# Performance work log

Hardware: AMD Instinct MI355X
Metric: run time of the kernel (lower is better)

Reference implementation:

```python
import jax, jax.numpy as jnp
import numpy as np

NUM_USER = 100000
NUM_ITEM = 50000
N = NUM_USER + NUM_ITEM
DIM_FEAT = 512
DIM_LATENT = 64
NNZ = 2400000
N_LAYERS = 3


def setup_inputs() -> dict:
    key = jax.random.key(0)
    ks = jax.random.split(key, 6)
    features = jax.random.normal(ks[0], (NUM_ITEM, DIM_FEAT), dtype=jnp.float32)
    user_id_preference = jax.random.normal(ks[1], (NUM_USER, DIM_LATENT), dtype=jnp.float32)
    W = jax.random.normal(ks[2], (DIM_FEAT, DIM_LATENT), dtype=jnp.float32) * (1.0 / np.sqrt(DIM_FEAT))
    b = jnp.zeros((DIM_LATENT,), dtype=jnp.float32)
    rows = jax.random.randint(ks[3], (NNZ,), 0, N, dtype=jnp.int32)
    cols = jax.random.randint(ks[4], (NNZ,), 0, N, dtype=jnp.int32)
    vals = jax.random.uniform(ks[5], (NNZ,), dtype=jnp.float32)
    return {"features": features, "user_id_preference": user_id_preference,
            "W": W, "b": b, "rows": rows, "cols": cols, "vals": vals}


def reference(features, user_id_preference, W, b, rows, cols, vals):
    # MLP projection of item features: [num_item, dim_latent]
    temp_features = features @ W + b
    # Concat user preferences and projected item features: [N, dim_latent]
    all_emb = jnp.concatenate([user_id_preference, temp_features], axis=0)
    # F.normalize: row-wise L2 normalization with eps=1e-12
    nrm = jnp.sqrt(jnp.sum(all_emb * all_emb, axis=1, keepdims=True))
    all_emb = all_emb / jnp.maximum(nrm, 1e-12)
    # 3-layer sparse propagation: out[r] += v * emb[c]; accumulate layer mean
    embs_sum = all_emb
    for _ in range(N_LAYERS):
        gathered = all_emb[cols] * vals[:, None]  # [nnz, dim_latent]
        all_emb = jax.ops.segment_sum(gathered, rows, num_segments=N)
        embs_sum = embs_sum + all_emb
    light_out = embs_sum / (N_LAYERS + 1)
    users = light_out[:NUM_USER]
    items = light_out[NUM_USER:]
    return (users, items)
```

## Files before the change

kernel.cpp:

```cpp
#include <hip/hip_runtime.h>

#define NUSER 100000
#define NITEM 50000
#define NTOT  150000
#define DF    512
#define DL    64
#define NNZ_  2400000
#define NB    1172
#define NCHUNK 256
#define CHUNK  9375

typedef short bf16x8 __attribute__((ext_vector_type(8)));
typedef float f32x4  __attribute__((ext_vector_type(4)));

__device__ __forceinline__ unsigned short bf16r(float f) {
    unsigned u = __float_as_uint(f);
    return (unsigned short)((u + 0x7FFFu + ((u >> 16) & 1u)) >> 16);
}
__device__ __forceinline__ unsigned pack2(float lo, float hi) {
    return (unsigned)bf16r(lo) | ((unsigned)bf16r(hi) << 16);
}

__global__ __launch_bounds__(256) void k_init(const float* __restrict__ up,
                                              const float* __restrict__ W,
                                              unsigned short* __restrict__ e0,
                                              unsigned short* __restrict__ Wtb) {
    int b = blockIdx.x;
    if (b < 128) {
        int idx = b * 256 + threadIdx.x;
        int k = idx >> 6, d = idx & 63;
        Wtb[d * DF + k] = bf16r(W[idx]);
        return;
    }
    int t = (b - 128) * 256 + threadIdx.x;
    float v = up[t];
    float ss = v * v;
    #pragma unroll
    for (int m = 32; m >= 1; m >>= 1) ss += __shfl_xor(ss, m, 64);
    float scale = 1.0f / fmaxf(sqrtf(ss), 1e-12f);
    e0[t] = bf16r(v * scale);
}

__global__ __launch_bounds__(256) void k_item(const float* __restrict__ F,
                                              const unsigned short* __restrict__ Wtb,
                                              const float* __restrict__ B,
                                              unsigned short* __restrict__ e0) {
    int t = threadIdx.x;
    int w = t >> 6, lane = t & 63;
    int g = lane >> 4;
    int c = lane & 15;
    int row_base = blockIdx.x * 64 + w * 16;

    int ar = row_base + c;
    if (ar >= NITEM) ar = NITEM - 1;
    const float* Frow = F + (size_t)ar * DF;

    f32x4 acc[4] = {};
    #pragma unroll 2
    for (int kc = 0; kc < DF; kc += 32) {
        int k0 = kc + g * 8;
        float4 f0 = *(const float4*)&Frow[k0];
        float4 f1 = *(const float4*)&Frow[k0 + 4];
        union { uint4 u; bf16x8 v; } a;
        a.u.x = pack2(f0.x, f0.y);
        a.u.y = pack2(f0.z, f0.w);
        a.u.z = pack2(f1.x, f1.y);
        a.u.w = pack2(f1.z, f1.w);
        #pragma unroll
        for (int ct = 0; ct < 4; ++ct) {
            union { uint4 u; bf16x8 v; } bb;
            bb.u = *(const uint4*)&Wtb[(size_t)(ct * 16 + c) * DF + k0];
            acc[ct] = __builtin_amdgcn_mfma_f32_16x16x32_bf16(a.v, bb.v, acc[ct], 0, 0, 0);
        }
    }

    #pragma unroll
    for (int ct = 0; ct < 4; ++ct) {
        float bc = B[ct * 16 + c];
        #pragma unroll
        for (int r = 0; r < 4; ++r) acc[ct][r] += bc;
    }
    float ssv[4];
    #pragma unroll
    for (int r = 0; r < 4; ++r) {
        float s = acc[0][r] * acc[0][r] + acc[1][r] * acc[1][r]
                + acc[2][r] * acc[2][r] + acc[3][r] * acc[3][r];
        #pragma unroll
        for (int m = 1; m <= 8; m <<= 1) s += __shfl_xor(s, m, 64);
        ssv[r] = 1.0f / fmaxf(sqrtf(s), 1e-12f);
    }
    #pragma unroll
    for (int r = 0; r < 4; ++r) {
        int gr = row_base + g * 4 + r;
        if (gr < NITEM) {
            size_t o = (size_t)(NUSER + gr) * DL + c;
            #pragma unroll
            for (int ct = 0; ct < 4; ++ct)
                e0[o + ct * 16] = bf16r(acc[ct][r] * ssv[r]);
        }
    }
}

__global__ __launch_bounds__(256) void k_hist(const int* __restrict__ rows,
                                              int* __restrict__ cnt) {
    __shared__ int h[NB];
    int c = blockIdx.x, t = threadIdx.x;
    for (int i = t; i < NB; i += 256) h[i] = 0;
    __syncthreads();
    int end = (c + 1) * CHUNK;
    for (int e = c * CHUNK + t; e < end; e += 256)
        atomicAdd(&h[rows[e] >> 7], 1);
    __syncthreads();
    for (int i = t; i < NB; i += 256) cnt[c * NB + i] = h[i];
}

__global__ __launch_bounds__(256) void k_scan1(const int* __restrict__ cnt,
                                               int* __restrict__ cntOff,
                                               int* __restrict__ binTot) {
    __shared__ int s[256];
    int b = blockIdx.x, t = threadIdx.x;
    int x = cnt[t * NB + b];
    s[t] = x;
    __syncthreads();
    #pragma unroll
    for (int off = 1; off < 256; off <<= 1) {
        int v = (t >= off) ? s[t - off] : 0;
        __syncthreads();
        s[t] += v;
        __syncthreads();
    }
    cntOff[t * NB + b] = s[t] - x;
    if (t == 255) binTot[b] = s[255];
}

__global__ __launch_bounds__(256) void k_scan2(const int* __restrict__ binTot,
                                               int* __restrict__ binBase) {
    __shared__ int s[256];
    __shared__ int carry;
    int t = threadIdx.x;
    if (t == 0) carry = 0;
    __syncthreads();
    for (int base = 0; base < NB; base += 256) {
        int idx = base + t;
        int x = (idx < NB) ? binTot[idx] : 0;
        s[t] = x;
        __syncthreads();
        #pragma unroll
        for (int off = 1; off < 256; off <<= 1) {
            int v = (t >= off) ? s[t - off] : 0;
            __syncthreads();
            s[t] += v;
            __syncthreads();
        }
        if (idx < NB) binBase[idx] = carry + s[t] - x;
        __syncthreads();
        if (t == 255) carry += s[255];
        __syncthreads();
    }
    if (t == 0) binBase[NB] = carry;
}

__global__ __launch_bounds__(256) void k_scatter(const int* __restrict__ rows,
                                                 const int* __restrict__ cols,
                                                 const float* __restrict__ vals,
                                                 const int* __restrict__ cntOff,
                                                 const int* __restrict__ binBase,
                                                 int2* __restrict__ eb) {
    __shared__ int cur[NB];
    int c = blockIdx.x, t = threadIdx.x;
    for (int i = t; i < NB; i += 256) cur[i] = binBase[i] + cntOff[c * NB + i];
    __syncthreads();
    int end = (c + 1) * CHUNK;
    for (int e = c * CHUNK + t; e < end; e += 256) {
        int r = rows[e];
        int b = r >> 7;
        int pos = atomicAdd(&cur[b], 1);
        eb[pos] = make_int2(cols[e] | ((r & 127) << 18), __float_as_int(vals[e]));
    }
}

__global__ __launch_bounds__(256) void k_binsort(const int2* __restrict__ eb,
                                                 const int* __restrict__ binBase,
                                                 int2* __restrict__ eb2,
                                                 int2* __restrict__ rowSC) {
    __shared__ int h[128];
    __shared__ int s[128];
    int b = blockIdx.x, t = threadIdx.x;
    if (t < 128) h[t] = 0;
    __syncthreads();
    int base = binBase[b];
    int cnt  = binBase[b + 1] - base;
    for (int j = t; j < cnt; j += 256)
        atomicAdd(&h[eb[base + j].x >> 18], 1);
    __syncthreads();
    if (t < 128) s[t] = h[t];
    __syncthreads();
    #pragma unroll
    for (int off = 1; off < 128; off <<= 1) {
        int v = 0;
        if (t < 128 && t >= off) v = s[t - off];
        __syncthreads();
        if (t < 128) s[t] += v;
        __syncthreads();
    }
    if (t < 128) {
        int e = s[t] - h[t];
        int r = (b << 7) + t;
        if (r < NTOT) rowSC[r] = make_int2(base + e, h[t]);
        s[t] = e;
    }
    __syncthreads();
    for (int j = t; j < cnt; j += 256) {
        int2 e = eb[base + j];
        int rl = e.x >> 18;
        int pos = base + atomicAdd(&s[rl], 1);
        eb2[pos] = make_int2(e.x & 0x3FFFF, e.y);
    }
}

__global__ __launch_bounds__(256) void k_spmm_row(const int2* __restrict__ rowSC,
                                                  const int2* __restrict__ eb2,
                                                  const unsigned short* __restrict__ embIn,
                                                  unsigned short* __restrict__ embOut) {
    int wid = (blockIdx.x * 256 + threadIdx.x) >> 6;
    if (wid >= NTOT) return;
    int lane = threadIdx.x & 63;
    int g = lane >> 3, ld = lane & 7;
    int2 sc = rowSC[wid];
    int j = sc.x + g;
    int end = sc.x + sc.y;
    float2 ac[4] = {};
    for (; j + 8 < end; j += 16) {
        int2 eA = eb2[j];
        int2 eB = eb2[j + 8];
        uint4 mA = *(const uint4*)&embIn[(size_t)eA.x * DL + ld * 8];
        uint4 mB = *(const uint4*)&embIn[(size_t)eB.x * DL + ld * 8];
        float vA = __int_as_float(eA.y), vB = __int_as_float(eB.y);
        const unsigned* pA = (const unsigned*)&mA;
        const unsigned* pB = (const unsigned*)&mB;
        #pragma unroll
        for (int k = 0; k < 4; ++k) {
            ac[k].x += vA * __uint_as_float(pA[k] << 16);
            ac[k].y += vA * __uint_as_float(pA[k] & 0xFFFF0000u);
            ac[k].x += vB * __uint_as_float(pB[k] << 16);
            ac[k].y += vB * __uint_as_float(pB[k] & 0xFFFF0000u);
        }
    }
    if (j < end) {
        int2 e = eb2[j];
        uint4 m = *(const uint4*)&embIn[(size_t)e.x * DL + ld * 8];
        float v = __int_as_float(e.y);
        const unsigned* p = (const unsigned*)&m;
        #pragma unroll
        for (int k = 0; k < 4; ++k) {
            ac[k].x += v * __uint_as_float(p[k] << 16);
            ac[k].y += v * __uint_as_float(p[k] & 0xFFFF0000u);
        }
    }
    float acc[8] = {ac[0].x, ac[0].y, ac[1].x, ac[1].y,
                    ac[2].x, ac[2].y, ac[3].x, ac[3].y};
    #pragma unroll
    for (int m = 8; m <= 32; m <<= 1) {
        #pragma unroll
        for (int k = 0; k < 8; ++k) acc[k] += __shfl_xor(acc[k], m, 64);
    }
    if (g == 0) {
        uint4 o;
        o.x = pack2(acc[0], acc[1]);
        o.y = pack2(acc[2], acc[3]);
        o.z = pack2(acc[4], acc[5]);
        o.w = pack2(acc[6], acc[7]);
        *(uint4*)&embOut[(size_t)wid * DL + ld * 8] = o;
    }
}

__global__ __launch_bounds__(256) void k_spmm_last(const int2* __restrict__ rowSC,
                                                   const int2* __restrict__ eb2,
                                                   const unsigned short* __restrict__ e0,
                                                   const unsigned short* __restrict__ e1,
                                                   const unsigned short* __restrict__ e2,
                                                   float* __restrict__ out) {
    int wid = (blockIdx.x * 256 + threadIdx.x) >> 6;
    if (wid >= NTOT) return;
    int lane = threadIdx.x & 63;
    int g = lane >> 3, ld = lane & 7;
    int2 sc = rowSC[wid];
    int j = sc.x + g;
    int end = sc.x + sc.y;
    float2 ac[4] = {};
    for (; j + 8 < end; j += 16) {
        int2 eA = eb2[j];
        int2 eB = eb2[j + 8];
        uint4 mA = *(const uint4*)&e2[(size_t)eA.x * DL + ld * 8];
        uint4 mB = *(const uint4*)&e2[(size_t)eB.x * DL + ld * 8];
        float vA = __int_as_float(eA.y), vB = __int_as_float(eB.y);
        const unsigned* pA = (const unsigned*)&mA;
        const unsigned* pB = (const unsigned*)&mB;
        #pragma unroll
        for (int k = 0; k < 4; ++k) {
            ac[k].x += vA * __uint_as_float(pA[k] << 16);
            ac[k].y += vA * __uint_as_float(pA[k] & 0xFFFF0000u);
            ac[k].x += vB * __uint_as_float(pB[k] << 16);
            ac[k].y += vB * __uint_as_float(pB[k] & 0xFFFF0000u);
        }
    }
    if (j < end) {
        int2 e = eb2[j];
        uint4 m = *(const uint4*)&e2[(size_t)e.x * DL + ld * 8];
        float v = __int_as_float(e.y);
        const unsigned* p = (const unsigned*)&m;
        #pragma unroll
        for (int k = 0; k < 4; ++k) {
            ac[k].x += v * __uint_as_float(p[k] << 16);
            ac[k].y += v * __uint_as_float(p[k] & 0xFFFF0000u);
        }
    }
    float acc[8] = {ac[0].x, ac[0].y, ac[1].x, ac[1].y,
                    ac[2].x, ac[2].y, ac[3].x, ac[3].y};
    #pragma unroll
    for (int m = 8; m <= 32; m <<= 1) {
        #pragma unroll
        for (int k = 0; k < 8; ++k) acc[k] += __shfl_xor(acc[k], m, 64);
    }
    if (g == 0) {
        size_t o = (size_t)wid * DL + ld * 8;
        uint4 a = *(const uint4*)&e0[o];
        uint4 b = *(const uint4*)&e1[o];
        uint4 c = *(const uint4*)&e2[o];
        const unsigned* pa = (const unsigned*)&a;
        const unsigned* pb = (const unsigned*)&b;
        const unsigned* pc = (const unsigned*)&c;
        float r[8];
        #pragma unroll
        for (int k = 0; k < 4; ++k) {
            float lo = __uint_as_float(pa[k] << 16) + __uint_as_float(pb[k] << 16)
                     + __uint_as_float(pc[k] << 16) + acc[2 * k];
            float hi = __uint_as_float(pa[k] & 0xFFFF0000u) + __uint_as_float(pb[k] & 0xFFFF0000u)
                     + __uint_as_float(pc[k] & 0xFFFF0000u) + acc[2 * k + 1];
            r[2 * k]     = 0.25f * lo;
            r[2 * k + 1] = 0.25f * hi;
        }
        *(float4*)&out[o]     = make_float4(r[0], r[1], r[2], r[3]);
        *(float4*)&out[o + 4] = make_float4(r[4], r[5], r[6], r[7]);
    }
}

extern "C" void kernel_launch(void* const* d_in, const int* in_sizes, int n_in,
                              void* d_out, int out_size, void* d_ws, size_t ws_size,
                              hipStream_t stream) {
    const float* F    = (const float*)d_in[0];
    const float* UP   = (const float*)d_in[1];
    const float* W    = (const float*)d_in[2];
    const float* B    = (const float*)d_in[3];
    const int*   rows = (const int*)d_in[4];
    const int*   cols = (const int*)d_in[5];
    const float* vals = (const float*)d_in[6];
    float* out = (float*)d_out;

    unsigned short* e0 = (unsigned short*)d_ws;
    unsigned short* e1 = e0 + (size_t)NTOT * DL;
    unsigned short* e2 = e1 + (size_t)NTOT * DL;
    int2* eb      = (int2*)(e2 + (size_t)NTOT * DL);
    int2* eb2     = eb + (size_t)NNZ_;
    int2* rowSC   = eb2 + (size_t)NNZ_;
    int*  cnt     = (int*)(rowSC + NTOT);
    int*  cntOff  = cnt + (size_t)NCHUNK * NB;
    int*  binTot  = cntOff + (size_t)NCHUNK * NB;
    int*  binBase = binTot + NB;
    unsigned short* Wtb = (unsigned short*)(binBase + NB + 1);

    k_init<<<128 + (NUSER * DL) / 256, 256, 0, stream>>>(UP, W, e0, Wtb);
    k_item<<<(NITEM + 63) / 64, 256, 0, stream>>>(F, Wtb, B, e0);
    k_hist<<<NCHUNK, 256, 0, stream>>>(rows, cnt);
    k_scan1<<<NB, 256, 0, stream>>>(cnt, cntOff, binTot);
    k_scan2<<<1, 256, 0, stream>>>(binTot, binBase);
    k_scatter<<<NCHUNK, 256, 0, stream>>>(rows, cols, vals, cntOff, binBase, eb);
    k_binsort<<<NB, 256, 0, stream>>>(eb, binBase, eb2, rowSC);

    k_spmm_row<<<(NTOT * DL) / 256, 256, 0, stream>>>(rowSC, eb2, e0, e1);
    k_spmm_row<<<(NTOT * DL) / 256, 256, 0, stream>>>(rowSC, eb2, e1, e2);
    k_spmm_last<<<(NTOT * DL) / 256, 256, 0, stream>>>(rowSC, eb2, e0, e1, e2, out);
}
```

Baseline: 356.5 us.

## Map each SpMM row to 16 lanes instead of a full wavefront

The three SpMM kernels now give each row to 16 threads, each owning 4 latent dims (8-byte bf16 loads), with 4-way unrolled serial iteration over the row's nonzeros. Before, a 64-lane wave split each row across 8 edge groups and then ran a shuffle reduction. The goal is to remove the cross-lane reduction and the idle lanes on rows with few nonzeros (about 16 per row on average), and to launch 4x fewer threads. The cost is narrower per-lane gathers and more serial dependence per row, which may reduce memory-level parallelism.

```diff
diff --git a/kernel.cpp b/kernel.cpp
--- a/kernel.cpp
+++ b/kernel.cpp
@@ -20,6 +20,8 @@
 __device__ __forceinline__ unsigned pack2(float lo, float hi) {
     return (unsigned)bf16r(lo) | ((unsigned)bf16r(hi) << 16);
 }
+__device__ __forceinline__ float blo(unsigned u) { return __uint_as_float(u << 16); }
+__device__ __forceinline__ float bhi(unsigned u) { return __uint_as_float(u & 0xFFFF0000u); }
 
 __global__ __launch_bounds__(256) void k_init(const float* __restrict__ up,
                                               const float* __restrict__ W,
@@ -222,56 +224,38 @@
                                                   const int2* __restrict__ eb2,
                                                   const unsigned short* __restrict__ embIn,
                                                   unsigned short* __restrict__ embOut) {
-    int wid = (blockIdx.x * 256 + threadIdx.x) >> 6;
-    if (wid >= NTOT) return;
-    int lane = threadIdx.x & 63;
-    int g = lane >> 3, ld = lane & 7;
-    int2 sc = rowSC[wid];
-    int j = sc.x + g;
-    int end = sc.x + sc.y;
-    float2 ac[4] = {};
-    for (; j + 8 < end; j += 16) {
-        int2 eA = eb2[j];
-        int2 eB = eb2[j + 8];
-        uint4 mA = *(const uint4*)&embIn[(size_t)eA.x * DL + ld * 8];
-        uint4 mB = *(const uint4*)&embIn[(size_t)eB.x * DL + ld * 8];
+    int gt = blockIdx.x * 256 + threadIdx.x;
+    int r  = gt >> 4;
+    if (r >= NTOT) return;
+    int lq = threadIdx.x & 15;
+    int2 sc = rowSC[r];
+    int j = sc.x, end = sc.x + sc.y;
+    float a0 = 0.f, a1 = 0.f, a2 = 0.f, a3 = 0.f;
+    int doff = lq * 4;
+    for (; j + 3 < end; j += 4) {
+        int2 eA = eb2[j],     eB = eb2[j + 1];
+        int2 eC = eb2[j + 2], eD = eb2[j + 3];
+        uint2 mA = *(const uint2*)&embIn[eA.x * DL + doff];
+        uint2 mB = *(const uint2*)&embIn[eB.x * DL + doff];
+        uint2 mC = *(const uint2*)&embIn[eC.x * DL + doff];
+        uint2 mD = *(const uint2*)&embIn[eD.x * DL + doff];
         float vA = __int_as_float(eA.y), vB = __int_as_float(eB.y);
-        const unsigned* pA = (const unsigned*)&mA;
-        const unsigned* pB = (const unsigned*)&mB;
-        #pragma unroll
-        for (int k = 0; k < 4; ++k) {
-            ac[k].x += vA * __uint_as_float(pA[k] << 16);
-            ac[k].y += vA * __uint_as_float(pA[k] & 0xFFFF0000u);
-            ac[k].x += vB * __uint_as_float(pB[k] << 16);
-            ac[k].y += vB * __uint_as_float(pB[k] & 0xFFFF0000u);
-        }
-    }
-    if (j < end) {
+        float vC = __int_as_float(eC.y), vD = __int_as_float(eD.y);
+        a0 += vA * blo(mA.x); a1 += vA * bhi(mA.x); a2 += vA * blo(mA.y); a3 += vA * bhi(mA.y);
+        a0 += vB * blo(mB.x); a1 += vB * bhi(mB.x); a2 += vB * blo(mB.y); a3 += vB * bhi(mB.y);
+        a0 += vC * blo(mC.x); a1 += vC * bhi(mC.x); a2 += vC * blo(mC.y); a3 += vC * bhi(mC.y);
+        a0 += vD * blo(mD.x); a1 += vD * bhi(mD.x); a2 += vD * blo(mD.y); a3 += vD * bhi(mD.y);
+    }
+    for (; j < end; ++j) {
         int2 e = eb2[j];
-        uint4 m = *(const uint4*)&embIn[(size_t)e.x * DL + ld * 8];
+        uint2 m = *(const uint2*)&embIn[e.x * DL + doff];
         float v = __int_as_float(e.y);
-        const unsigned* p = (const unsigned*)&m;
-        #pragma unroll
-        for (int k = 0; k < 4; ++k) {
-            ac[k].x += v * __uint_as_float(p[k] << 16);
-            ac[k].y += v * __uint_as_float(p[k] & 0xFFFF0000u);
-        }
-    }
-    float acc[8] = {ac[0].x, ac[0].y, ac[1].x, ac[1].y,
-                    ac[2].x, ac[2].y, ac[3].x, ac[3].y};
-    #pragma unroll
-    for (int m = 8; m <= 32; m <<= 1) {
-        #pragma unroll
-        for (int k = 0; k < 8; ++k) acc[k] += __shfl_xor(acc[k], m, 64);
-    }
-    if (g == 0) {
-        uint4 o;
-        o.x = pack2(acc[0], acc[1]);
-        o.y = pack2(acc[2], acc[3]);
-        o.z = pack2(acc[4], acc[5]);
-        o.w = pack2(acc[6], acc[7]);
-        *(uint4*)&embOut[(size_t)wid * DL + ld * 8] = o;
-    }
+        a0 += v * blo(m.x); a1 += v * bhi(m.x); a2 += v * blo(m.y); a3 += v * bhi(m.y);
+    }
+    uint2 o;
+    o.x = pack2(a0, a1);
+    o.y = pack2(a2, a3);
+    *(uint2*)&embOut[r * DL + doff] = o;
 }
 
 __global__ __launch_bounds__(256) void k_spmm_last(const int2* __restrict__ rowSC,
@@ -280,69 +264,44 @@
                                                    const unsigned short* __restrict__ e1,
                                                    const unsigned short* __restrict__ e2,
                                                    float* __restrict__ out) {
-    int wid = (blockIdx.x * 256 + threadIdx.x) >> 6;
-    if (wid >= NTOT) return;
-    int lane = threadIdx.x & 63;
-    int g = lane >> 3, ld = lane & 7;
-    int2 sc = rowSC[wid];
-    int j = sc.x + g;
-    int end = sc.x + sc.y;
-    float2 ac[4] = {};
-    for (; j + 8 < end; j += 16) {
-        int2 eA = eb2[j];
-        int2 eB = eb2[j + 8];
-        uint4 mA = *(const uint4*)&e2[(size_t)eA.x * DL + ld * 8];
-        uint4 mB = *(const uint4*)&e2[(size_t)eB.x * DL + ld * 8];
+    int gt = blockIdx.x * 256 + threadIdx.x;
+    int r  = gt >> 4;
+    if (r >= NTOT) return;
+    int lq = threadIdx.x & 15;
+    int2 sc = rowSC[r];
+    int j = sc.x, end = sc.x + sc.y;
+    float a0 = 0.f, a1 = 0.f, a2 = 0.f, a3 = 0.f;
+    int doff = lq * 4;
+    for (; j + 3 < end; j += 4) {
+        int2 eA = eb2[j],     eB = eb2[j + 1];
+        int2 eC = eb2[j + 2], eD = eb2[j + 3];
+        uint2 mA = *(const uint2*)&e2[eA.x * DL + doff];
+        uint2 mB = *(const uint2*)&e2[eB.x * DL + doff];
+        uint2 mC = *(const uint2*)&e2[eC.x * DL + doff];
+        uint2 mD = *(const uint2*)&e2[eD.x * DL + doff];
         float vA = __int_as_float(eA.y), vB = __int_as_float(eB.y);
-        const unsigned* pA = (const unsigned*)&mA;
-        const unsigned* pB = (const unsigned*)&mB;
-        #pragma unroll
-        for (int k = 0; k < 4; ++k) {
-            ac[k].x += vA * __uint_as_float(pA[k] << 16);
-            ac[k].y += vA * __uint_as_float(pA[k] & 0xFFFF0000u);
-            ac[k].x += vB * __uint_as_float(pB[k] << 16);
-            ac[k].y += vB * __uint_as_float(pB[k] & 0xFFFF0000u);
-        }
-    }
-    if (j < end) {
+        float vC = __int_as_float(eC.y), vD = __int_as_float(eD.y);
+        a0 += vA * blo(mA.x); a1 += vA * bhi(mA.x); a2 += vA * blo(mA.y); a3 += vA * bhi(mA.y);
+        a0 += vB * blo(mB.x); a1 += vB * bhi(mB.x); a2 += vB * blo(mB.y); a3 += vB * bhi(mB.y);
+        a0 += vC * blo(mC.x); a1 += vC * bhi(mC.x); a2 += vC * blo(mC.y); a3 += vC * bhi(mC.y);
+        a0 += vD * blo(mD.x); a1 += vD * bhi(mD.x); a2 += vD * blo(mD.y); a3 += vD * bhi(mD.y);
+    }
+    for (; j < end; ++j) {
         int2 e = eb2[j];
-        uint4 m = *(const uint4*)&e2[(size_t)e.x * DL + ld * 8];
+        uint2 m = *(const uint2*)&e2[e.x * DL + doff];
         float v = __int_as_float(e.y);
-        const unsigned* p = (const unsigned*)&m;
-        #pragma unroll
-        for (int k = 0; k < 4; ++k) {
-            ac[k].x += v * __uint_as_float(p[k] << 16);
-            ac[k].y += v * __uint_as_float(p[k] & 0xFFFF0000u);
-        }
-    }
-    float acc[8] = {ac[0].x, ac[0].y, ac[1].x, ac[1].y,
-                    ac[2].x, ac[2].y, ac[3].x, ac[3].y};
-    #pragma unroll
-    for (int m = 8; m <= 32; m <<= 1) {
-        #pragma unroll
-        for (int k = 0; k < 8; ++k) acc[k] += __shfl_xor(acc[k], m, 64);
-    }
-    if (g == 0) {
-        size_t o = (size_t)wid * DL + ld * 8;
-        uint4 a = *(const uint4*)&e0[o];
-        uint4 b = *(const uint4*)&e1[o];
-        uint4 c = *(const uint4*)&e2[o];
-        const unsigned* pa = (const unsigned*)&a;
-        const unsigned* pb = (const unsigned*)&b;
-        const unsigned* pc = (const unsigned*)&c;
-        float r[8];
-        #pragma unroll
-        for (int k = 0; k < 4; ++k) {
-            float lo = __uint_as_float(pa[k] << 16) + __uint_as_float(pb[k] << 16)
-                     + __uint_as_float(pc[k] << 16) + acc[2 * k];
-            float hi = __uint_as_float(pa[k] & 0xFFFF0000u) + __uint_as_float(pb[k] & 0xFFFF0000u)
-                     + __uint_as_float(pc[k] & 0xFFFF0000u) + acc[2 * k + 1];
-            r[2 * k]     = 0.25f * lo;
-            r[2 * k + 1] = 0.25f * hi;
-        }
-        *(float4*)&out[o]     = make_float4(r[0], r[1], r[2], r[3]);
-        *(float4*)&out[o + 4] = make_float4(r[4], r[5], r[6], r[7]);
-    }
+        a0 += v * blo(m.x); a1 += v * bhi(m.x); a2 += v * blo(m.y); a3 += v * bhi(m.y);
+    }
+    int o = r * DL + doff;
+    uint2 ua = *(const uint2*)&e0[o];
+    uint2 ub = *(const uint2*)&e1[o];
+    uint2 uc = *(const uint2*)&e2[o];
+    float4 res;
+    res.x = 0.25f * (blo(ua.x) + blo(ub.x) + blo(uc.x) + a0);
+    res.y = 0.25f * (bhi(ua.x) + bhi(ub.x) + bhi(uc.x) + a1);
+    res.z = 0.25f * (blo(ua.y) + blo(ub.y) + blo(uc.y) + a2);
+    res.w = 0.25f * (bhi(ua.y) + bhi(ub.y) + bhi(uc.y) + a3);
+    *(float4*)&out[o] = res;
 }
 
 extern "C" void kernel_launch(void* const* d_in, const int* in_sizes, int n_in,
@@ -377,7 +336,8 @@
     k_scatter<<<NCHUNK, 256, 0, stream>>>(rows, cols, vals, cntOff, binBase, eb);
     k_binsort<<<NB, 256, 0, stream>>>(eb, binBase, eb2, rowSC);
 
-    k_spmm_row<<<(NTOT * DL) / 256, 256, 0, stream>>>(rowSC, eb2, e0, e1);
-    k_spmm_row<<<(NTOT * DL) / 256, 256, 0, stream>>>(rowSC, eb2, e1, e2);
-    k_spmm_last<<<(NTOT * DL) / 256, 256, 0, stream>>>(rowSC, eb2, e0, e1, e2, out);
-}
+    int spmm_blocks = (NTOT * 16 + 255) / 256;
+    k_spmm_row<<<spmm_blocks, 256, 0, stream>>>(rowSC, eb2, e0, e1);
+    k_spmm_row<<<spmm_blocks, 256, 0, stream>>>(rowSC, eb2, e1, e2);
+    k_spmm_last<<<spmm_blocks, 256, 0, stream>>>(rowSC, eb2, e0, e1, e2, out);
+}
```

Measured after the change: 338.9 us. 1.05x faster.
